# Optimization experiments

Hardware: AMD Instinct MI355X
Metric: run time of the kernel (lower is better)

## Reference

```python
import jax, jax.numpy as jnp
import numpy as np

DEPTH = 4
CH = 3
SIG_CHANNELS = 3 + 9 + 27 + 81  # signatory.signature_channels(3, 4) = 120


def _tp(a, b):
    # flattened tensor (outer) product: (N, p) x (N, q) -> (N, p*q), row-major (signatory ordering)
    return (a[:, :, None] * b[:, None, :]).reshape(a.shape[0], -1)


def _signature(path):
    """Depth-4 path signature of path: (N, T, 3) -> (N, 120).

    Segment signature of a linear piece with increment dx is exp(dx):
    levels dx^{otimes k} / k!. Segments are combined with Chen's identity
    via a lax.scan over the time axis.
    """
    dx = path[:, 1:, :] - path[:, :-1, :]  # (N, T-1, 3)
    N, Tm1, _ = dx.shape
    dt = path.dtype
    # per-segment signature levels (flattened)
    s1 = dx                                                                # (N,T-1,3)
    s2 = (s1[..., :, None] * dx[..., None, :]).reshape(N, Tm1, 9) / 2.0   # dx^2/2!
    s3 = (s2[..., :, None] * dx[..., None, :]).reshape(N, Tm1, 27) / 3.0  # dx^3/3!
    s4 = (s3[..., :, None] * dx[..., None, :]).reshape(N, Tm1, 81) / 4.0  # dx^4/4!
    segs = (jnp.moveaxis(s1, 1, 0), jnp.moveaxis(s2, 1, 0),
            jnp.moveaxis(s3, 1, 0), jnp.moveaxis(s4, 1, 0))  # time-leading for scan

    init = (jnp.zeros((N, 3), dt), jnp.zeros((N, 9), dt),
            jnp.zeros((N, 27), dt), jnp.zeros((N, 81), dt))

    def chen_step(carry, seg):
        c1, c2, c3, c4 = carry
        g1, g2, g3, g4 = seg
        n1 = c1 + g1
        n2 = c2 + _tp(c1, g1) + g2
        n3 = c3 + _tp(c2, g1) + _tp(c1, g2) + g3
        n4 = c4 + _tp(c3, g1) + _tp(c2, g2) + _tp(c1, g3) + g4
        return (n1, n2, n3, n4), None

    (c1, c2, c3, c4), _ = jax.lax.scan(chen_step, init, segs)
    return jnp.concatenate([c1, c2, c3, c4], axis=1)  # (N, 120)


def setup_inputs() -> dict:
    key = jax.random.key(0)
    k1, k2, k3, k4, k5 = jax.random.split(key, 5)
    B, T, V, M = 64, 300, 17, 2
    inp = jax.random.normal(k1, (B, CH, T, V, M), dtype=jnp.float32)
    fan1 = 34 * SIG_CHANNELS  # 4080
    W1 = jax.random.uniform(k2, (512, fan1), jnp.float32, -1.0, 1.0) / np.sqrt(fan1)
    b1 = jax.random.uniform(k3, (512,), jnp.float32, -1.0, 1.0) / np.sqrt(fan1)
    W2 = jax.random.uniform(k4, (155, 512), jnp.float32, -1.0, 1.0) / np.sqrt(512)
    b2 = jax.random.uniform(k5, (155,), jnp.float32, -1.0, 1.0) / np.sqrt(512)
    return {"inp": inp, "W1": W1, "b1": b1, "W2": W2, "b2": b2}


def reference(inp, W1, b1, W2, b2):
    B, _, T, V, M = inp.shape
    # order matches the torch loop: for v in range(17): for m in range(2)
    paths = jnp.transpose(inp, (0, 3, 4, 2, 1)).reshape(B * V * M, T, CH)  # (B*34, T, 3)
    sig = _signature(paths).reshape(B, V * M * SIG_CHANNELS)  # (B, 4080)
    h = sig @ W1.T + b1  # dropout is identity in eval mode
    return h @ W2.T + b2  # (B, 155)
```

## Files before the change

kernel.cpp:

```cpp
#include <hip/hip_runtime.h>
#include <hip/hip_bf16.h>

#define B_SZ 64
#define T_PTS 300
#define N_SEG 299
#define VM 34
#define NPATH (B_SZ*VM)
#define SIGC 120
#define FAN1 4080
#define H1 512
#define NOUT 155
#define GSZ 16
#define CHUNK 19
#define TT 75
#define KSPL 48
#define KW 85

__device__ __forceinline__ void sig_append(float a1[3], float a2[9], float a3[27], float a4[81],
                                           float d0, float d1, float d2) {
  float B1[3] = {d0, d1, d2};
  float Hh[3] = {0.5f * d0, 0.5f * d1, 0.5f * d2};
  float Tt[3] = {(1.0f / 3.0f) * d0, (1.0f / 3.0f) * d1, (1.0f / 3.0f) * d2};
  float Qq[3] = {0.25f * d0, 0.25f * d1, 0.25f * d2};
  float B2[9], B3[27];
#pragma unroll
  for (int i = 0; i < 3; i++)
#pragma unroll
    for (int j = 0; j < 3; j++) B2[i * 3 + j] = B1[i] * Hh[j];
#pragma unroll
  for (int e = 0; e < 27; e++) B3[e] = B2[e / 3] * Tt[e % 3];

#pragma unroll
  for (int e = 0; e < 81; e++) {
    float v = a4[e];
    v = fmaf(B3[e / 3], Qq[e % 3], v);
    v = fmaf(a3[e / 3], B1[e % 3], v);
    v = fmaf(a2[e / 9], B2[e % 9], v);
    v = fmaf(a1[e / 27], B3[e % 27], v);
    a4[e] = v;
  }
#pragma unroll
  for (int e = 0; e < 27; e++) {
    float v = a3[e] + B3[e];
    v = fmaf(a2[e / 3], B1[e % 3], v);
    v = fmaf(a1[e / 9], B2[e % 9], v);
    a3[e] = v;
  }
#pragma unroll
  for (int e = 0; e < 9; e++) a2[e] = fmaf(a1[e / 3], B1[e % 3], a2[e] + B2[e]);
  a1[0] += d0; a1[1] += d1; a1[2] += d2;
}

__global__ __launch_bounds__(256) void transpose_kernel(const float* __restrict__ inp,
                                                        float* __restrict__ tp,
                                                        const float* __restrict__ b1,
                                                        float* __restrict__ ht) {
  const int b = blockIdx.x;
  const int tile = blockIdx.y;
  const int t0 = tile * TT;
  const int tid = threadIdx.x;
  __shared__ float lds[3 * TT * VM];

  const float* src = inp + (size_t)b * 3 * T_PTS * VM;
  for (int idx = tid; idx < 3 * TT * VM; idx += 256) {
    const int c = idx / (TT * VM);
    const int rem = idx - c * (TT * VM);
    lds[idx] = src[(c * T_PTS + t0) * VM + rem];
  }
  __syncthreads();

  for (int idx = tid; idx < VM * TT * 3; idx += 256) {
    const int vm = idx / (TT * 3);
    const int i = idx - vm * (TT * 3);
    const int tt = i / 3;
    const int c = i - tt * 3;
    tp[((size_t)(b * VM + vm) * T_PTS + t0 + tt) * 3 + c] = lds[(c * TT + tt) * VM + vm];
  }

  if (tile == 0) {
    for (int idx = tid; idx < 8 * 64; idx += 256)
      ht[(size_t)(8 * b) * 64 + idx] = b1[8 * b + (idx >> 6)];
  }
}

__global__ __launch_bounds__(64)
__attribute__((amdgpu_waves_per_eu(1, 1)))
void sig_kernel(const float* __restrict__ tp, float* __restrict__ St) {
  const int lane = threadIdx.x & 63;
  const int g = lane >> 4;
  const int sub = lane & (GSZ - 1);
  const int p = blockIdx.x * 4 + g;
  const int t0 = sub * CHUNK;

  const float* bp = tp + (size_t)p * (T_PTS * 3) + t0 * 3;

  float a1[3], a2[9], a3[27], a4[81];
#pragma unroll
  for (int i = 0; i < 3; i++) a1[i] = 0.f;
#pragma unroll
  for (int i = 0; i < 9; i++) a2[i] = 0.f;
#pragma unroll
  for (int i = 0; i < 27; i++) a3[i] = 0.f;
#pragma unroll
  for (int i = 0; i < 81; i++) a4[i] = 0.f;

  float x0 = bp[0], x1 = bp[1], x2 = bp[2];
  for (int s = 0; s < CHUNK; s++) {
    const float y0 = bp[3 * s + 3];
    const float y1 = bp[3 * s + 4];
    const float y2 = bp[3 * s + 5];
    const bool valid = (t0 + s) < N_SEG;
    const float d0 = valid ? (y0 - x0) : 0.0f;
    const float d1 = valid ? (y1 - x1) : 0.0f;
    const float d2 = valid ? (y2 - x2) : 0.0f;
    sig_append(a1, a2, a3, a4, d0, d1, d2);
    x0 = y0; x1 = y1; x2 = y2;
  }

#pragma unroll
  for (int off = 1; off < GSZ; off <<= 1) {
    const float m = (sub + off < GSZ) ? 1.0f : 0.0f;
    float B1[3], B2[9], B3[27];
#pragma unroll
    for (int i = 0; i < 3; i++) B1[i] = m * __shfl_down(a1[i], off);
#pragma unroll
    for (int i = 0; i < 9; i++) B2[i] = m * __shfl_down(a2[i], off);
#pragma unroll
    for (int i = 0; i < 27; i++) B3[i] = m * __shfl_down(a3[i], off);

#pragma unroll
    for (int e = 0; e < 81; e++) {
      const float b4 = m * __shfl_down(a4[e], off);
      float v = a4[e] + b4;
      v = fmaf(a3[e / 3], B1[e % 3], v);
      v = fmaf(a2[e / 9], B2[e % 9], v);
      v = fmaf(a1[e / 27], B3[e % 27], v);
      a4[e] = v;
    }
#pragma unroll
    for (int e = 0; e < 27; e++) {
      float v = a3[e] + B3[e];
      v = fmaf(a2[e / 3], B1[e % 3], v);
      v = fmaf(a1[e / 9], B2[e % 9], v);
      a3[e] = v;
    }
#pragma unroll
    for (int e = 0; e < 9; e++) a2[e] = fmaf(a1[e / 3], B1[e % 3], a2[e] + B2[e]);
#pragma unroll
    for (int i = 0; i < 3; i++) a1[i] += B1[i];
  }

  if (sub == 0) {
    const int b = p / VM;
    const int vm = p - b * VM;
    float* dst = St + (size_t)(vm * SIGC) * 64 + b;
#pragma unroll
    for (int i = 0; i < 3; i++) dst[(size_t)i * 64] = a1[i];
#pragma unroll
    for (int i = 0; i < 9; i++) dst[(size_t)(3 + i) * 64] = a2[i];
#pragma unroll
    for (int i = 0; i < 27; i++) dst[(size_t)(12 + i) * 64] = a3[i];
#pragma unroll
    for (int i = 0; i < 81; i++) dst[(size_t)(39 + i) * 64] = a4[i];
  }
}

__global__ __launch_bounds__(256) void gemm1_kernel(const float* __restrict__ St,
                                                    const float* __restrict__ W1,
                                                    float* __restrict__ ht) {
  const int lane = threadIdx.x & 63;
  int wave_id = (blockIdx.x * 256 + threadIdx.x) >> 6;
  wave_id = __builtin_amdgcn_readfirstlane(wave_id);
  const int ks = wave_id / 128;
  const int jg = wave_id & 127;
  const int k0 = ks * KW;

  const float* stp = St + (size_t)k0 * 64 + lane;
  const float* w0 = W1 + (size_t)(jg * 4 + 0) * FAN1 + k0;
  const float* w1 = W1 + (size_t)(jg * 4 + 1) * FAN1 + k0;
  const float* w2 = W1 + (size_t)(jg * 4 + 2) * FAN1 + k0;
  const float* w3 = W1 + (size_t)(jg * 4 + 3) * FAN1 + k0;

  float sv[KW];
#pragma unroll
  for (int i = 0; i < KW; i++) sv[i] = stp[(size_t)i * 64];

  float acc0 = 0.f, acc1 = 0.f, acc2 = 0.f, acc3 = 0.f;
#pragma unroll
  for (int i = 0; i < KW; i++) {
    acc0 = fmaf(sv[i], w0[i], acc0);
    acc1 = fmaf(sv[i], w1[i], acc1);
    acc2 = fmaf(sv[i], w2[i], acc2);
    acc3 = fmaf(sv[i], w3[i], acc3);
  }

  float* hp = ht + (size_t)(jg * 4) * 64 + lane;
  atomicAdd(hp + 0 * 64, acc0);
  atomicAdd(hp + 1 * 64, acc1);
  atomicAdd(hp + 2 * 64, acc2);
  atomicAdd(hp + 3 * 64, acc3);
}

__global__ __launch_bounds__(256) void gemm2_kernel(const float* __restrict__ ht,
                                                    const float* __restrict__ W2,
                                                    const float* __restrict__ b2,
                                                    float* __restrict__ out) {
  const int j = blockIdx.x;
  const int lane = threadIdx.x & 63;
  int w = threadIdx.x >> 6;
  w = __builtin_amdgcn_readfirstlane(w);
  __shared__ float red[4][64];

  const float* htp = ht + (size_t)(w * 128) * 64 + lane;
  const float* w2r = W2 + (size_t)j * H1 + w * 128;
  float acc = 0.f;
#pragma unroll 8
  for (int k = 0; k < 128; k++) acc = fmaf(w2r[k], htp[(size_t)k * 64], acc);

  red[w][lane] = acc;
  __syncthreads();
  if (threadIdx.x < 64) {
    const float tot = red[0][lane] + red[1][lane] + red[2][lane] + red[3][lane];
    out[(size_t)lane * NOUT + j] = tot + b2[j];
  }
}

extern "C" void kernel_launch(void* const* d_in, const int* in_sizes, int n_in,
                              void* d_out, int out_size, void* d_ws, size_t ws_size,
                              hipStream_t stream) {
  const float* inp = (const float*)d_in[0];
  const float* W1  = (const float*)d_in[1];
  const float* b1  = (const float*)d_in[2];
  const float* W2  = (const float*)d_in[3];
  const float* b2  = (const float*)d_in[4];
  float* out = (float*)d_out;

  float* tpbuf = (float*)d_ws;
  float* St    = tpbuf + (size_t)NPATH * T_PTS * 3;
  float* ht    = St + (size_t)FAN1 * 64;

  transpose_kernel<<<dim3(B_SZ, 4), 256, 0, stream>>>(inp, tpbuf, b1, ht);
  sig_kernel<<<NPATH / 4, 64, 0, stream>>>(tpbuf, St);
  gemm1_kernel<<<KSPL * 128 / 4, 256, 0, stream>>>(St, W1, ht);
  gemm2_kernel<<<NOUT, 256, 0, stream>>>(ht, W2, b2, out);
}
```

Baseline: 119.8 us.

## Pad sig kernel LDS to cap occupancy and stream shuffles in tree reduction

Adds a 40KB volatile shared-memory pad to sig_kernel so fewer blocks share a compute unit, giving each wave more register and cache room. It also reorders the cross-lane Chen combine so shuffled values are fetched and used at once instead of being staged in full B2/B3 arrays, which cuts live registers and spilling. The cost is extra shuffles, since a2 and a3 entries are shuffled more than once, and the forced occupancy limit could reduce latency hiding.

```diff
diff --git a/kernel.cpp b/kernel.cpp
--- a/kernel.cpp
+++ b/kernel.cpp
@@ -86,6 +86,9 @@
 __global__ __launch_bounds__(64)
 __attribute__((amdgpu_waves_per_eu(1, 1)))
 void sig_kernel(const float* __restrict__ tp, float* __restrict__ St) {
+  volatile __shared__ float occ_pad[10240];
+  occ_pad[threadIdx.x] = 0.0f;
+
   const int lane = threadIdx.x & 63;
   const int g = lane >> 4;
   const int sub = lane & (GSZ - 1);
@@ -120,34 +123,45 @@
 #pragma unroll
   for (int off = 1; off < GSZ; off <<= 1) {
     const float m = (sub + off < GSZ) ? 1.0f : 0.0f;
-    float B1[3], B2[9], B3[27];
-#pragma unroll
-    for (int i = 0; i < 3; i++) B1[i] = m * __shfl_down(a1[i], off);
-#pragma unroll
-    for (int i = 0; i < 9; i++) B2[i] = m * __shfl_down(a2[i], off);
-#pragma unroll
-    for (int i = 0; i < 27; i++) B3[i] = m * __shfl_down(a3[i], off);
-
-#pragma unroll
-    for (int e = 0; e < 81; e++) {
-      const float b4 = m * __shfl_down(a4[e], off);
-      float v = a4[e] + b4;
-      v = fmaf(a3[e / 3], B1[e % 3], v);
-      v = fmaf(a2[e / 9], B2[e % 9], v);
-      v = fmaf(a1[e / 27], B3[e % 27], v);
-      a4[e] = v;
+    float b1v[3];
+#pragma unroll
+    for (int i = 0; i < 3; i++) b1v[i] = m * __shfl_down(a1[i], off);
+
+#pragma unroll
+    for (int lo = 0; lo < 27; lo++) {
+      const float b3v = m * __shfl_down(a3[lo], off);
+      const float b2v = m * __shfl_down(a2[lo % 9], off);
+#pragma unroll
+      for (int hi = 0; hi < 3; hi++) {
+        const int e = 27 * hi + lo;
+        const float b4v = m * __shfl_down(a4[e], off);
+        float v = a4[e] + b4v;
+        v = fmaf(a3[9 * hi + lo / 3], b1v[lo % 3], v);
+        v = fmaf(a2[3 * hi + lo / 9], b2v, v);
+        v = fmaf(a1[hi], b3v, v);
+        a4[e] = v;
+      }
     }
 #pragma unroll
-    for (int e = 0; e < 27; e++) {
-      float v = a3[e] + B3[e];
-      v = fmaf(a2[e / 3], B1[e % 3], v);
-      v = fmaf(a1[e / 9], B2[e % 9], v);
-      a3[e] = v;
+    for (int lo = 0; lo < 9; lo++) {
+      const float b2v = m * __shfl_down(a2[lo], off);
+#pragma unroll
+      for (int hi = 0; hi < 3; hi++) {
+        const int e = 9 * hi + lo;
+        const float b3v = m * __shfl_down(a3[e], off);
+        float v = a3[e] + b3v;
+        v = fmaf(a2[3 * hi + lo / 3], b1v[lo % 3], v);
+        v = fmaf(a1[hi], b2v, v);
+        a3[e] = v;
+      }
     }
 #pragma unroll
-    for (int e = 0; e < 9; e++) a2[e] = fmaf(a1[e / 3], B1[e % 3], a2[e] + B2[e]);
-#pragma unroll
-    for (int i = 0; i < 3; i++) a1[i] += B1[i];
+    for (int e = 0; e < 9; e++) {
+      const float b2v = m * __shfl_down(a2[e], off);
+      a2[e] = fmaf(a1[e / 3], b1v[e % 3], a2[e] + b2v);
+    }
+#pragma unroll
+    for (int i = 0; i < 3; i++) a1[i] += b1v[i];
   }
 
   if (sub == 0) {
```

After: 121.9 us. Within noise of the previous version (+1.7%).
